# Performance work log

Hardware: AMD Instinct MI355X
Metric: run time of the kernel (lower is better)

## Reference

```python
import jax, jax.numpy as jnp
import numpy as np

HID = 3584
NH = 28
NKV = 4
HD = HID // NH  # 128
T = 2048
THETA = 1000000.0
SCALE = HD ** -0.5


def setup_inputs() -> dict:
    key = jax.random.key(0)
    ks = jax.random.split(key, 9)
    s = 0.02
    return {
        "positions": jnp.arange(T, dtype=jnp.int32),
        "hidden_states": jax.random.normal(ks[0], (T, HID), dtype=jnp.float32),
        "wq": jax.random.normal(ks[1], (HID, NH * HD), dtype=jnp.float32) * s,
        "bq": jax.random.normal(ks[2], (NH * HD,), dtype=jnp.float32) * s,
        "wk": jax.random.normal(ks[3], (HID, NKV * HD), dtype=jnp.float32) * s,
        "bk": jax.random.normal(ks[4], (NKV * HD,), dtype=jnp.float32) * s,
        "wv": jax.random.normal(ks[5], (HID, NKV * HD), dtype=jnp.float32) * s,
        "bv": jax.random.normal(ks[6], (NKV * HD,), dtype=jnp.float32) * s,
        "wo": jax.random.normal(ks[7], (NH * HD, HID), dtype=jnp.float32) * s,
    }


def _rope(x, positions):
    # neox-style RoPE over full head_dim: split halves, rotate.
    half = HD // 2
    inv_freq = 1.0 / (THETA ** (jnp.arange(0, half, dtype=jnp.float32) / half))
    ang = positions.astype(jnp.float32)[:, None] * inv_freq  # [T, half]
    cos = jnp.cos(ang)[:, None, :]  # [T, 1, half]
    sin = jnp.sin(ang)[:, None, :]
    x1, x2 = x[..., :half], x[..., half:]
    return jnp.concatenate([x1 * cos - x2 * sin, x2 * cos + x1 * sin], axis=-1)


def reference(positions, hidden_states, wq, bq, wk, bk, wv, bv, wo):
    q = (hidden_states @ wq + bq).reshape(T, NH, HD)
    k = (hidden_states @ wk + bk).reshape(T, NKV, HD)
    v = (hidden_states @ wv + bv).reshape(T, NKV, HD)
    q = _rope(q, positions)
    k = _rope(k, positions)
    # GQA: expand kv heads to query heads (groups of NH//NKV)
    g = NH // NKV
    k = jnp.repeat(k, g, axis=1)  # [T, NH, HD]
    v = jnp.repeat(v, g, axis=1)
    scores = jnp.einsum("thd,shd->hts", q, k) * SCALE  # bidirectional, no mask
    probs = jax.nn.softmax(scores, axis=-1)
    attn = jnp.einsum("hts,shd->thd", probs, v).reshape(T, NH * HD)
    return attn @ wo
```

## Files before the change

### kernel.cpp

```cpp
#include <hip/hip_runtime.h>

typedef __bf16 bf16_t;
typedef __attribute__((ext_vector_type(8))) __bf16 bf16x8;
typedef __attribute__((ext_vector_type(4))) float floatx4;

#define T_SEQ 2048
#define HID 3584
#define NH 28
#define NKV 4
#define HD 128
#define GQA 7
#define SCALE_F 0.08838834764831845f
#define QSCALE_LOG2 0.1275179100693744f

__global__ void conv_bf_k(const float* __restrict__ src, bf16_t* __restrict__ dst, long n) {
  const long i = ((long)blockIdx.x * 256 + threadIdx.x) * 8;
  if (i >= n) return;
  const floatx4 a = *(const floatx4*)(src + i);
  const floatx4 b = *(const floatx4*)(src + i + 4);
  bf16x8 r;
  r[0] = (bf16_t)a[0]; r[1] = (bf16_t)a[1]; r[2] = (bf16_t)a[2]; r[3] = (bf16_t)a[3];
  r[4] = (bf16_t)b[0]; r[5] = (bf16_t)b[1]; r[6] = (bf16_t)b[2]; r[7] = (bf16_t)b[3];
  *(bf16x8*)(dst + i) = r;
}

__global__ __launch_bounds__(256) void tconv_k(const float* __restrict__ src,
                                               bf16_t* __restrict__ dst, long N, long K) {
  __shared__ alignas(16) bf16_t t[64][72];
  const long k0 = (long)blockIdx.y * 64, n0 = (long)blockIdx.x * 64;
  const int tid = threadIdx.x;
  const int rr = tid >> 4;
  const int cc = (tid & 15) * 4;
#pragma unroll
  for (int i = 0; i < 4; ++i) {
    const int r = rr + i * 16;
    const floatx4 v = *(const floatx4*)(src + (k0 + r) * N + n0 + cc);
#pragma unroll
    for (int j = 0; j < 4; ++j) t[cc + j][r] = (bf16_t)v[j];
  }
  __syncthreads();
#pragma unroll
  for (int i = 0; i < 2; ++i) {
    const int J = i * 256 + tid;
    const int n = J >> 3, c8 = (J & 7) * 8;
    *(bf16x8*)(dst + (n0 + n) * K + k0 + c8) = *(const bf16x8*)(&t[n][c8]);
  }
}

__device__ __forceinline__ bf16x8 ld8(const void* p, long idx, bool f32) {
  if (f32) {
    const float* q = (const float*)p + idx;
    const floatx4 u = *(const floatx4*)q;
    const floatx4 v = *(const floatx4*)(q + 4);
    bf16x8 r;
    r[0] = (bf16_t)u[0]; r[1] = (bf16_t)u[1]; r[2] = (bf16_t)u[2]; r[3] = (bf16_t)u[3];
    r[4] = (bf16_t)v[0]; r[5] = (bf16_t)v[1]; r[6] = (bf16_t)v[2]; r[7] = (bf16_t)v[3];
    return r;
  }
  return *(const bf16x8*)((const bf16_t*)p + idx);
}

__device__ __forceinline__ void gld16(const bf16_t* g, bf16_t* l) {
  __builtin_amdgcn_global_load_lds(
      (const __attribute__((address_space(1))) unsigned int*)(const void*)g,
      (__attribute__((address_space(3))) unsigned int*)(void*)l, 16, 0, 0);
}

__global__ __launch_bounds__(256) void gemm_bt_k(
    const bf16_t* __restrict__ A, long lda,
    const bf16_t* __restrict__ Bt, long ldb,
    const float* __restrict__ bias, void* Cv, long ldc,
    int K, int mode, void* Cv2) {
  __shared__ alignas(16) bf16_t ldsA[2][128 * 32];
  __shared__ alignas(16) bf16_t ldsB[2][128 * 32];
  const int tid = threadIdx.x;
  const int lane = tid & 63;
  const int w = tid >> 6;
  const int wr = w >> 1, wc = w & 1;
  const int col = lane & 15, quad = lane >> 4;
  const long m0 = (long)blockIdx.y * 128, n0 = (long)blockIdx.x * 128;

  const int r0 = tid >> 2;
  const int c0 = tid & 3;
  const int cs = c0 ^ ((r0 >> 1) & 3);
  const int r1 = 64 + r0;

  const bf16_t* Ab = A + m0 * lda + cs * 8;
  const bf16_t* Bb = Bt + n0 * ldb + cs * 8;

  floatx4 acc[4][4] = {};
  const int nt = K >> 5;

  auto stage = [&](int buf, int t) {
    const long k0 = (long)t << 5;
    gld16(Ab + (long)r0 * lda + k0, ldsA[buf] + tid * 8);
    gld16(Ab + (long)r1 * lda + k0, ldsA[buf] + (256 + tid) * 8);
    gld16(Bb + (long)r0 * ldb + k0, ldsB[buf] + tid * 8);
    gld16(Bb + (long)r1 * ldb + k0, ldsB[buf] + (256 + tid) * 8);
  };

  stage(0, 0);
  for (int t = 0; t < nt; ++t) {
    const int cur = t & 1;
    stage(cur ^ 1, (t + 1 == nt) ? 0 : t + 1);
    __builtin_amdgcn_sched_barrier(0);
    asm volatile("s_waitcnt vmcnt(4)" ::: "memory");
    __builtin_amdgcn_sched_barrier(0);
    __builtin_amdgcn_s_barrier();
    __builtin_amdgcn_sched_barrier(0);
    bf16x8 af[4], bf[4];
#pragma unroll
    for (int i = 0; i < 4; ++i) {
      const int ra = wr * 64 + i * 16 + col;
      af[i] = *(const bf16x8*)(ldsA[cur] + ra * 32 + (quad ^ ((ra >> 1) & 3)) * 8);
    }
#pragma unroll
    for (int j = 0; j < 4; ++j) {
      const int rb = wc * 64 + j * 16 + col;
      bf[j] = *(const bf16x8*)(ldsB[cur] + rb * 32 + (quad ^ ((rb >> 1) & 3)) * 8);
    }
#pragma unroll
    for (int i = 0; i < 4; ++i)
#pragma unroll
      for (int j = 0; j < 4; ++j)
        acc[i][j] = __builtin_amdgcn_mfma_f32_16x16x32_bf16(af[i], bf[j], acc[i][j], 0, 0, 0);
    __builtin_amdgcn_sched_barrier(0);
    __builtin_amdgcn_s_barrier();
    __builtin_amdgcn_sched_barrier(0);
  }

#pragma unroll
  for (int i = 0; i < 4; ++i) {
#pragma unroll
    for (int j = 0; j < 4; ++j) {
      const long row0 = m0 + wr * 64 + i * 16 + quad * 4;
      const long cc = n0 + wc * 64 + j * 16 + col;
      const float bvv = bias ? bias[cc] : 0.f;
#pragma unroll
      for (int r = 0; r < 4; ++r) {
        const float v = acc[i][j][r] + bvv;
        if (mode == 0)      ((bf16_t*)Cv)[(row0 + r) * ldc + cc] = (bf16_t)v;
        else if (mode == 1) ((float*)Cv)[(row0 + r) * ldc + cc] = v;
        else {
          if (cc < 3584)      ((bf16_t*)Cv)[(row0 + r) * ldc + cc] = (bf16_t)v;
          else if (cc < 4096) ((bf16_t*)Cv2)[(row0 + r) * 512 + (cc - 3584)] = (bf16_t)v;
          else ((bf16_t*)Cv2)[1048576 + (cc - 4096) * (long)T_SEQ + (row0 + r)] = (bf16_t)v;
        }
      }
    }
  }
}

__global__ __launch_bounds__(256) void gemm_nt_k(
    const void* A, long lda, const void* B, long ldb,
    const float* bias, void* Cv, long ldc,
    int K, int aMode, int bMode, int transC, int c32, const int* flag) {
  __shared__ alignas(16) bf16_t ldsA[128 * 32];
  __shared__ alignas(16) unsigned int ldsB32[128 * 16];
  const int f = *flag;
  const bool aF32 = aMode && (f > 32);
  const bool bF32 = bMode && (f > 32);
  const int tid = threadIdx.x;
  const int lane = tid & 63;
  const int w = tid >> 6;
  const int wr = w >> 1, wc = w & 1;
  const int col = lane & 15, quad = lane >> 4;
  const long m0 = (long)blockIdx.y * 128, n0 = (long)blockIdx.x * 128;

  const int ar1 = tid >> 2, ak = (tid & 3) * 8;
  const int ar2 = 64 + ar1;
  const int kk = (tid >> 4) * 2;
  const int nn = (tid & 15) * 8;
  const int kp = kk >> 1;

  floatx4 acc[4][4] = {};

  for (int k0 = 0; k0 < K; k0 += 32) {
    const bf16x8 a1 = ld8(A, (m0 + ar1) * lda + k0 + ak, aF32);
    const bf16x8 a2 = ld8(A, (m0 + ar2) * lda + k0 + ak, aF32);
    const bf16x8 b0 = ld8(B, (long)(k0 + kk) * ldb + n0 + nn, bF32);
    const bf16x8 b1 = ld8(B, (long)(k0 + kk + 1) * ldb + n0 + nn, bF32);
    __syncthreads();
    *(bf16x8*)(ldsA + ar1 * 32 + ak) = a1;
    *(bf16x8*)(ldsA + ar2 * 32 + ak) = a2;
#pragma unroll
    for (int j = 0; j < 8; ++j) {
      const int n = nn + j;
      const int pk = ((((kp >> 2) ^ ((n >> 3) & 3)) << 2) | (kp & 3));
      union { struct { bf16_t lo, hi; } s; unsigned int u; } cv;
      cv.s.lo = b0[j];
      cv.s.hi = b1[j];
      ldsB32[n * 16 + pk] = cv.u;
    }
    __syncthreads();
    bf16x8 af[4], bfv[4];
#pragma unroll
    for (int i = 0; i < 4; ++i)
      af[i] = *(const bf16x8*)(ldsA + (wr * 64 + i * 16 + col) * 32 + quad * 8);
#pragma unroll
    for (int j = 0; j < 4; ++j) {
      const int n = wc * 64 + j * 16 + col;
      const int blk = quad ^ ((n >> 3) & 3);
      bfv[j] = *(const bf16x8*)((const bf16_t*)(ldsB32 + n * 16 + blk * 4));
    }
#pragma unroll
    for (int i = 0; i < 4; ++i)
#pragma unroll
      for (int jj = 0; jj < 4; ++jj)
        acc[i][jj] = __builtin_amdgcn_mfma_f32_16x16x32_bf16(af[i], bfv[jj], acc[i][jj], 0, 0, 0);
  }

#pragma unroll
  for (int i = 0; i < 4; ++i) {
#pragma unroll
    for (int j = 0; j < 4; ++j) {
      const long row0 = m0 + wr * 64 + i * 16 + quad * 4;
      const long cc = n0 + wc * 64 + j * 16 + col;
      const float bvv = bias ? bias[cc] : 0.f;
#pragma unroll
      for (int r = 0; r < 4; ++r) {
        const float v = acc[i][j][r] + bvv;
        if (transC)   ((bf16_t*)Cv)[cc * ldc + (row0 + r)] = (bf16_t)v;
        else if (c32) ((float*)Cv)[(row0 + r) * ldc + cc] = v;
        else          ((bf16_t*)Cv)[(row0 + r) * ldc + cc] = (bf16_t)v;
      }
    }
  }
}

__global__ void rope_k(bf16_t* buf, const int* __restrict__ pos, long ld, int nheads) {
  const int idx = blockIdx.x * 256 + threadIdx.x;
  const int total = T_SEQ * nheads * 64;
  if (idx >= total) return;
  const int d = idx & 63;
  const int th = idx >> 6;
  const int h = th % nheads;
  const int t = th / nheads;
  const float inv = exp2f((float)d * (-19.931568569324174f / 64.f));
  const float ang = (float)pos[t] * inv;
  float sn, cs;
  __sincosf(ang, &sn, &cs);
  bf16_t* p = buf + (long)t * ld + h * HD + d;
  const float x1 = (float)p[0];
  const float x2 = (float)p[64];
  p[0] = (bf16_t)(x1 * cs - x2 * sn);
  p[64] = (bf16_t)(x2 * cs + x1 * sn);
}

__global__ __launch_bounds__(256, 2) void attn5_k(
    const bf16_t* __restrict__ q, long qs,
    const bf16_t* __restrict__ k, long ks,
    const bf16_t* __restrict__ vt,
    bf16_t* __restrict__ out, long os) {
  __shared__ alignas(16) bf16_t ldsK[2][64 * 128];
  __shared__ alignas(16) bf16_t ldsV[2][128 * 64];
  __shared__ alignas(16) bf16_t pbuf[4][32 * 64];

  const int h = blockIdx.y;
  const long hkvHD = (long)(h / GQA) * HD;
  const int tid = threadIdx.x;
  const int lane = tid & 63;
  const int w = tid >> 6;
  const int col = lane & 15, quad = lane >> 4;
  const int t0 = blockIdx.x * 128 + w * 32;

  auto stage = [&](int buf, int t) {
    const long s0 = (long)t * 64;
#pragma unroll
    for (int i = 0; i < 4; ++i) {
      const int J = i * 256 + tid;
      {
        const int row = J >> 4;
        const int cs = (J & 15) ^ (row & 7);
        gld16(k + (s0 + row) * ks + hkvHD + cs * 8, &ldsK[buf][J * 8]);
      }
      {
        const int row = J >> 3;
        const int cs = (J & 7) ^ (row & 7);
        gld16(vt + (hkvHD + row) * T_SEQ + s0 + cs * 8, &ldsV[buf][J * 8]);
      }
    }
  };

  bf16x8 aq[2][4];
#pragma unroll
  for (int sub = 0; sub < 2; ++sub) {
    const bf16_t* qp = q + (long)(t0 + sub * 16 + col) * qs + h * HD + quad * 8;
#pragma unroll
    for (int c = 0; c < 4; ++c) {
      aq[sub][c] = *(const bf16x8*)(qp + c * 32);
#pragma unroll
      for (int e = 0; e < 8; ++e)
        aq[sub][c][e] = (bf16_t)((float)aq[sub][c][e] * QSCALE_LOG2);
    }
  }

  bf16x8 ones;
#pragma unroll
  for (int e = 0; e < 8; ++e) ones[e] = (bf16_t)1.0f;

  floatx4 O[2][8] = {};
  float m_w[2] = {-1e30f, -1e30f};
  float l_i[2][4] = {};

  stage(0, 0);
  for (int t = 0; t < 32; ++t) {
    const int cur = t & 1;
    stage(cur ^ 1, (t + 1) & 31);
    __builtin_amdgcn_sched_barrier(0);
    asm volatile("s_waitcnt vmcnt(8)" ::: "memory");
    __builtin_amdgcn_sched_barrier(0);
    __builtin_amdgcn_s_barrier();
    __builtin_amdgcn_sched_barrier(0);

    floatx4 S[2][4] = {};
    __builtin_amdgcn_s_setprio(1);
#pragma unroll
    for (int nt = 0; nt < 4; ++nt) {
      const int row = nt * 16 + col;
#pragma unroll
      for (int c = 0; c < 4; ++c) {
        const int cs = (c * 4 + quad) ^ (row & 7);
        const bf16x8 bk = *(const bf16x8*)(&ldsK[cur][row * 128 + cs * 8]);
        S[0][nt] = __builtin_amdgcn_mfma_f32_16x16x32_bf16(aq[0][c], bk, S[0][nt], 0, 0, 0);
        S[1][nt] = __builtin_amdgcn_mfma_f32_16x16x32_bf16(aq[1][c], bk, S[1][nt], 0, 0, 0);
      }
    }
    __builtin_amdgcn_s_setprio(0);

#pragma unroll
    for (int sub = 0; sub < 2; ++sub) {
      float mx = S[sub][0][0];
#pragma unroll
      for (int nt = 0; nt < 4; ++nt)
#pragma unroll
        for (int r = 0; r < 4; ++r) mx = fmaxf(mx, S[sub][nt][r]);
#pragma unroll
      for (int off = 1; off < 64; off <<= 1)
        mx = fmaxf(mx, __shfl_xor(mx, off, 64));
      if (mx > m_w[sub] + 12.0f) {
        const float alpha = exp2f(m_w[sub] - mx);
        m_w[sub] = mx;
#pragma unroll
        for (int r = 0; r < 4; ++r) l_i[sub][r] *= alpha;
#pragma unroll
        for (int dt = 0; dt < 8; ++dt)
#pragma unroll
          for (int r = 0; r < 4; ++r) O[sub][dt][r] *= alpha;
      }
    }

#pragma unroll
    for (int sub = 0; sub < 2; ++sub)
#pragma unroll
      for (int r = 0; r < 4; ++r) {
        const int mrow = sub * 16 + quad * 4 + r;
#pragma unroll
        for (int nt = 0; nt < 4; ++nt) {
          const float p = exp2f(S[sub][nt][r] - m_w[sub]);
          const int cs = (nt * 2 + (col >> 3)) ^ (mrow & 7);
          pbuf[w][mrow * 64 + cs * 8 + (col & 7)] = (bf16_t)p;
        }
      }

    floatx4 Ssum[2] = {};
    __builtin_amdgcn_s_setprio(1);
#pragma unroll
    for (int kb = 0; kb < 2; ++kb) {
      const int csp = (kb * 4 + quad) ^ (col & 7);
      const bf16x8 pa0 = *(const bf16x8*)(&pbuf[w][(col) * 64 + csp * 8]);
      const bf16x8 pa1 = *(const bf16x8*)(&pbuf[w][(16 + col) * 64 + csp * 8]);
      Ssum[0] = __builtin_amdgcn_mfma_f32_16x16x32_bf16(pa0, ones, Ssum[0], 0, 0, 0);
      Ssum[1] = __builtin_amdgcn_mfma_f32_16x16x32_bf16(pa1, ones, Ssum[1], 0, 0, 0);
#pragma unroll
      for (int dt = 0; dt < 8; ++dt) {
        const int vrow = dt * 16 + col;
        const bf16x8 bv = *(const bf16x8*)(&ldsV[cur][vrow * 64 + csp * 8]);
        O[0][dt] = __builtin_amdgcn_mfma_f32_16x16x32_bf16(pa0, bv, O[0][dt], 0, 0, 0);
        O[1][dt] = __builtin_amdgcn_mfma_f32_16x16x32_bf16(pa1, bv, O[1][dt], 0, 0, 0);
      }
    }
    __builtin_amdgcn_s_setprio(0);
#pragma unroll
    for (int sub = 0; sub < 2; ++sub)
#pragma unroll
      for (int r = 0; r < 4; ++r) l_i[sub][r] += Ssum[sub][r];

    __builtin_amdgcn_sched_barrier(0);
    __builtin_amdgcn_s_barrier();
    __builtin_amdgcn_sched_barrier(0);
  }

#pragma unroll
  for (int sub = 0; sub < 2; ++sub) {
#pragma unroll
    for (int r = 0; r < 4; ++r) l_i[sub][r] = 1.f / l_i[sub][r];
#pragma unroll
    for (int dt = 0; dt < 8; ++dt) {
#pragma unroll
      for (int r = 0; r < 4; ++r) {
        const long trow = t0 + sub * 16 + quad * 4 + r;
        out[trow * os + h * HD + dt * 16 + col] = (bf16_t)(O[sub][dt][r] * l_i[sub][r]);
      }
    }
  }
}

extern "C" void kernel_launch(void* const* d_in, const int* in_sizes, int n_in,
                              void* d_out_v, int out_size, void* d_ws, size_t ws_size,
                              hipStream_t stream) {
  const int* pos = (const int*)d_in[0];
  const float* hidden = (const float*)d_in[1];
  const float* wq = (const float*)d_in[2];
  const float* bq = (const float*)d_in[3];
  const float* wk = (const float*)d_in[4];
  const float* bk = (const float*)d_in[5];
  const float* wv = (const float*)d_in[6];
  const float* bv = (const float*)d_in[7];
  const float* wo = (const float*)d_in[8];

  bf16_t* qbuf = (bf16_t*)d_out_v;
  bf16_t* attn_hi = (bf16_t*)d_out_v + (size_t)T_SEQ * HID;
  float* outf = (float*)d_out_v;

  char* ws = (char*)d_ws;
  const size_t NEED = 51904516;

  if (ws_size >= NEED) {
    bf16_t* hbf  = (bf16_t*)ws;
    bf16_t* wqbt = (bf16_t*)(ws + 14680064);
    bf16_t* wkbt = (bf16_t*)(ws + 40370176);
    bf16_t* wvbt = (bf16_t*)(ws + 44040192);
    bf16_t* kbuf = (bf16_t*)(ws + 47710208);
    bf16_t* vt   = (bf16_t*)(ws + 49807360);
    bf16_t* wobt = wqbt;
    bf16_t* attnb = hbf;
    float* bqkv = (float*)attn_hi;

    hipMemcpyAsync(bqkv, bq, 3584 * sizeof(float), hipMemcpyDeviceToDevice, stream);
    hipMemcpyAsync(bqkv + 3584, bk, 512 * sizeof(float), hipMemcpyDeviceToDevice, stream);
    hipMemcpyAsync(bqkv + 4096, bv, 512 * sizeof(float), hipMemcpyDeviceToDevice, stream);

    conv_bf_k<<<3584, 256, 0, stream>>>(hidden, hbf, (long)T_SEQ * HID);
    tconv_k<<<dim3(56, 56), 256, 0, stream>>>(wq, wqbt, HID, HID);
    tconv_k<<<dim3(8, 56), 256, 0, stream>>>(wk, wkbt, 512, HID);
    tconv_k<<<dim3(8, 56), 256, 0, stream>>>(wv, wvbt, 512, HID);

    gemm_bt_k<<<dim3(36, 16), 256, 0, stream>>>(hbf, HID, wqbt, HID, bqkv, qbuf, HID,
                                                HID, 3, kbuf);

    rope_k<<<(T_SEQ * NH * 64) / 256, 256, 0, stream>>>(qbuf, pos, HID, NH);
    rope_k<<<(T_SEQ * NKV * 64) / 256, 256, 0, stream>>>(kbuf, pos, 512, NKV);

    attn5_k<<<dim3(16, 28), 256, 0, stream>>>(qbuf, HID, kbuf, 512, vt, attnb, HID);

    tconv_k<<<dim3(56, 56), 256, 0, stream>>>(wo, wobt, HID, HID);

    gemm_bt_k<<<dim3(28, 16), 256, 0, stream>>>(attnb, HID, wobt, HID, nullptr,
                                                outf, HID, HID, 1, nullptr);
  } else {
    bf16_t* kbuf = (bf16_t*)ws;
    bf16_t* vt = (bf16_t*)(ws + 2097152);
    bf16_t* acopy = (bf16_t*)ws;
    int* flag = (int*)(ws + 4194304);

    hipMemsetAsync(flag, 64, 4, stream);

    gemm_nt_k<<<dim3(28, 16), 256, 0, stream>>>(hidden, HID, wq, HID, bq, qbuf, HID,
                                                HID, 1, 1, 0, 0, flag);
    gemm_nt_k<<<dim3(4, 16), 256, 0, stream>>>(hidden, HID, wk, 512, bk, kbuf, 512,
                                               HID, 1, 1, 0, 0, flag);
    gemm_nt_k<<<dim3(4, 16), 256, 0, stream>>>(hidden, HID, wv, 512, bv, vt, T_SEQ,
                                               HID, 1, 1, 1, 0, flag);

    rope_k<<<(T_SEQ * NH * 64) / 256, 256, 0, stream>>>(qbuf, pos, HID, NH);
    rope_k<<<(T_SEQ * NKV * 64) / 256, 256, 0, stream>>>(kbuf, pos, 512, NKV);

    attn5_k<<<dim3(16, 28), 256, 0, stream>>>(qbuf, HID, kbuf, 512, vt, attn_hi, HID);

    hipMemcpyAsync(acopy, attn_hi + (size_t)1536 * HID, (size_t)512 * HID * 2,
                   hipMemcpyDeviceToDevice, stream);
    gemm_nt_k<<<dim3(28, 8), 256, 0, stream>>>(attn_hi, HID, wo, HID, nullptr,
                                               outf, HID, HID, 0, 1, 0, 1, flag);
    gemm_nt_k<<<dim3(28, 4), 256, 0, stream>>>(attn_hi + (size_t)1024 * HID, HID, wo, HID,
                                               nullptr, outf + (size_t)1024 * HID, HID,
                                               HID, 0, 1, 0, 1, flag);
    gemm_nt_k<<<dim3(28, 4), 256, 0, stream>>>(acopy, HID, wo, HID,
                                               nullptr, outf + (size_t)1536 * HID, HID,
                                               HID, 0, 1, 0, 1, flag);
  }
}
```

Baseline: 502.6 us.

## Enlarge projection GEMM tiles to 256x256x64 with eight waves per block

Replaces the 128x128 bf16 GEMM with a 256x256 tile, K-step 64, eight waves each computing 128x64, with an 8-way XOR LDS swizzle and raised wave priority around the MFMA block. It aims to increase data reuse per LDS load and cut global traffic per flop. The grids shrink to 144 and 112 blocks, fewer than the CU count, and the 128KB LDS footprint limits residency to one block per CU, which risks underusing the GPU.

```diff
diff --git a/kernel.cpp b/kernel.cpp
--- a/kernel.cpp
+++ b/kernel.cpp
@@ -66,37 +66,34 @@
       (__attribute__((address_space(3))) unsigned int*)(void*)l, 16, 0, 0);
 }
 
-__global__ __launch_bounds__(256) void gemm_bt_k(
+__global__ __launch_bounds__(512, 2) void gemm8_k(
     const bf16_t* __restrict__ A, long lda,
     const bf16_t* __restrict__ Bt, long ldb,
     const float* __restrict__ bias, void* Cv, long ldc,
     int K, int mode, void* Cv2) {
-  __shared__ alignas(16) bf16_t ldsA[2][128 * 32];
-  __shared__ alignas(16) bf16_t ldsB[2][128 * 32];
+  __shared__ alignas(16) bf16_t ldsA[2][256 * 64];
+  __shared__ alignas(16) bf16_t ldsB[2][256 * 64];
   const int tid = threadIdx.x;
   const int lane = tid & 63;
   const int w = tid >> 6;
-  const int wr = w >> 1, wc = w & 1;
+  const int wr = w >> 2;
+  const int wcn = w & 3;
   const int col = lane & 15, quad = lane >> 4;
-  const long m0 = (long)blockIdx.y * 128, n0 = (long)blockIdx.x * 128;
-
-  const int r0 = tid >> 2;
-  const int c0 = tid & 3;
-  const int cs = c0 ^ ((r0 >> 1) & 3);
-  const int r1 = 64 + r0;
-
-  const bf16_t* Ab = A + m0 * lda + cs * 8;
-  const bf16_t* Bb = Bt + n0 * ldb + cs * 8;
-
-  floatx4 acc[4][4] = {};
-  const int nt = K >> 5;
+  const long m0 = (long)blockIdx.y * 256, n0 = (long)blockIdx.x * 256;
+
+  floatx4 acc[8][4] = {};
+  const int nt = K >> 6;
 
   auto stage = [&](int buf, int t) {
-    const long k0 = (long)t << 5;
-    gld16(Ab + (long)r0 * lda + k0, ldsA[buf] + tid * 8);
-    gld16(Ab + (long)r1 * lda + k0, ldsA[buf] + (256 + tid) * 8);
-    gld16(Bb + (long)r0 * ldb + k0, ldsB[buf] + tid * 8);
-    gld16(Bb + (long)r1 * ldb + k0, ldsB[buf] + (256 + tid) * 8);
+    const long kk = (long)t << 6;
+#pragma unroll
+    for (int i = 0; i < 4; ++i) {
+      const int cj = i * 512 + tid;
+      const int row = cj >> 3;
+      const int sc = (cj & 7) ^ (row & 7);
+      gld16(A + (m0 + row) * lda + kk + sc * 8, ldsA[buf] + cj * 8);
+      gld16(Bt + (n0 + row) * ldb + kk + sc * 8, ldsB[buf] + cj * 8);
+    }
   };
 
   stage(0, 0);
@@ -104,41 +101,48 @@
     const int cur = t & 1;
     stage(cur ^ 1, (t + 1 == nt) ? 0 : t + 1);
     __builtin_amdgcn_sched_barrier(0);
-    asm volatile("s_waitcnt vmcnt(4)" ::: "memory");
+    asm volatile("s_waitcnt vmcnt(8)" ::: "memory");
     __builtin_amdgcn_sched_barrier(0);
     __builtin_amdgcn_s_barrier();
     __builtin_amdgcn_sched_barrier(0);
-    bf16x8 af[4], bf[4];
-#pragma unroll
-    for (int i = 0; i < 4; ++i) {
-      const int ra = wr * 64 + i * 16 + col;
-      af[i] = *(const bf16x8*)(ldsA[cur] + ra * 32 + (quad ^ ((ra >> 1) & 3)) * 8);
-    }
-#pragma unroll
-    for (int j = 0; j < 4; ++j) {
-      const int rb = wc * 64 + j * 16 + col;
-      bf[j] = *(const bf16x8*)(ldsB[cur] + rb * 32 + (quad ^ ((rb >> 1) & 3)) * 8);
-    }
-#pragma unroll
-    for (int i = 0; i < 4; ++i)
-#pragma unroll
-      for (int j = 0; j < 4; ++j)
-        acc[i][j] = __builtin_amdgcn_mfma_f32_16x16x32_bf16(af[i], bf[j], acc[i][j], 0, 0, 0);
+
+#pragma unroll
+    for (int ks = 0; ks < 2; ++ks) {
+      bf16x8 af[8], bf[4];
+#pragma unroll
+      for (int m = 0; m < 8; ++m) {
+        const int ra = wr * 128 + m * 16 + col;
+        af[m] = *(const bf16x8*)(ldsA[cur] + ra * 64 + (((ks << 2) | quad) ^ (ra & 7)) * 8);
+      }
+#pragma unroll
+      for (int n = 0; n < 4; ++n) {
+        const int rb = wcn * 64 + n * 16 + col;
+        bf[n] = *(const bf16x8*)(ldsB[cur] + rb * 64 + (((ks << 2) | quad) ^ (rb & 7)) * 8);
+      }
+      __builtin_amdgcn_s_setprio(1);
+#pragma unroll
+      for (int m = 0; m < 8; ++m)
+#pragma unroll
+        for (int n = 0; n < 4; ++n)
+          acc[m][n] = __builtin_amdgcn_mfma_f32_16x16x32_bf16(af[m], bf[n], acc[m][n], 0, 0, 0);
+      __builtin_amdgcn_s_setprio(0);
+    }
+
     __builtin_amdgcn_sched_barrier(0);
     __builtin_amdgcn_s_barrier();
     __builtin_amdgcn_sched_barrier(0);
   }
 
 #pragma unroll
-  for (int i = 0; i < 4; ++i) {
-#pragma unroll
-    for (int j = 0; j < 4; ++j) {
-      const long row0 = m0 + wr * 64 + i * 16 + quad * 4;
-      const long cc = n0 + wc * 64 + j * 16 + col;
+  for (int m = 0; m < 8; ++m) {
+#pragma unroll
+    for (int n = 0; n < 4; ++n) {
+      const long row0 = m0 + wr * 128 + m * 16 + quad * 4;
+      const long cc = n0 + wcn * 64 + n * 16 + col;
       const float bvv = bias ? bias[cc] : 0.f;
 #pragma unroll
       for (int r = 0; r < 4; ++r) {
-        const float v = acc[i][j][r] + bvv;
+        const float v = acc[m][n][r] + bvv;
         if (mode == 0)      ((bf16_t*)Cv)[(row0 + r) * ldc + cc] = (bf16_t)v;
         else if (mode == 1) ((float*)Cv)[(row0 + r) * ldc + cc] = v;
         else {
@@ -446,8 +450,8 @@
     tconv_k<<<dim3(8, 56), 256, 0, stream>>>(wk, wkbt, 512, HID);
     tconv_k<<<dim3(8, 56), 256, 0, stream>>>(wv, wvbt, 512, HID);
 
-    gemm_bt_k<<<dim3(36, 16), 256, 0, stream>>>(hbf, HID, wqbt, HID, bqkv, qbuf, HID,
-                                                HID, 3, kbuf);
+    gemm8_k<<<dim3(18, 8), 512, 0, stream>>>(hbf, HID, wqbt, HID, bqkv, qbuf, HID,
+                                             HID, 3, kbuf);
 
     rope_k<<<(T_SEQ * NH * 64) / 256, 256, 0, stream>>>(qbuf, pos, HID, NH);
     rope_k<<<(T_SEQ * NKV * 64) / 256, 256, 0, stream>>>(kbuf, pos, 512, NKV);
@@ -456,8 +460,8 @@
 
     tconv_k<<<dim3(56, 56), 256, 0, stream>>>(wo, wobt, HID, HID);
 
-    gemm_bt_k<<<dim3(28, 16), 256, 0, stream>>>(attnb, HID, wobt, HID, nullptr,
-                                                outf, HID, HID, 1, nullptr);
+    gemm8_k<<<dim3(14, 8), 512, 0, stream>>>(attnb, HID, wobt, HID, nullptr,
+                                             outf, HID, HID, 1, nullptr);
   } else {
     bf16_t* kbuf = (bf16_t*)ws;
     bf16_t* vt = (bf16_t*)(ws + 2097152);
```

Result: slower. 578.9 us (+15.2%).
